# Performance work log

Hardware: AMD Instinct MI355X
Metric: run time of the kernel (lower is better)

The kernel has to match this reference:

```python
import jax, jax.numpy as jnp
import numpy as np

BITS = 4
NPACK = 32 // BITS            # 8 nibbles per int32
GROUPSIZE = 128
IN_F = 8192
OUT_F = 8192
BATCH = 64
NGROUPS = IN_F // GROUPSIZE   # 64
MASK = (1 << BITS) - 1        # 15


def setup_inputs() -> dict:
    key = jax.random.key(0)
    k1, k2, k3, k4, k5 = jax.random.split(key, 5)
    x = jax.random.normal(k1, (BATCH, IN_F), dtype=jnp.float32)
    qweight = jax.random.randint(k2, (IN_F // NPACK, OUT_F), 0, 2**31 - 1, dtype=jnp.int32)
    qzeros = jax.random.randint(k3, (NGROUPS, OUT_F // NPACK), 0, 2**31 - 1, dtype=jnp.int32)
    scales = jax.random.uniform(k4, (NGROUPS, OUT_F), dtype=jnp.float32, minval=1e-3, maxval=1e-2)
    bias = jax.random.normal(k5, (OUT_F,), dtype=jnp.float32)
    return {"x": x, "qweight": qweight, "qzeros": qzeros, "scales": scales, "bias": bias}


def _dequantize(qweight, qzeros, scales):
    shifts = (jnp.arange(NPACK, dtype=jnp.int32) * BITS)
    # unpack weight nibbles along in_features: [in/8, 8, out] -> [in, out]
    w = (qweight[:, None, :] >> shifts[None, :, None]) & MASK
    w = w.reshape(IN_F, OUT_F).astype(jnp.float32)
    # unpack zero points along out_features: [g, out/8, 8] -> [g, out]
    zp = (qzeros[:, :, None] >> shifts[None, None, :]) & MASK
    zp = zp.reshape(NGROUPS, OUT_F) + 1                       # optimum format stores zp-1
    zp = jnp.where(zp > MASK, 0, zp).astype(jnp.float32)      # wraparound per recover()
    g_idx = jnp.arange(IN_F) // GROUPSIZE                     # per-input-channel group id
    return (w - zp[g_idx]) * scales[g_idx]                    # [in, out] fp weight


def reference(x, qweight, qzeros, scales, bias):
    W = _dequantize(qweight, qzeros, scales)                  # [in, out]
    return x @ W + bias                                       # F.linear(x, W.T, bias)
```

## Files before the change

kernel.cpp:

```cpp
#include <hip/hip_runtime.h>
#include <hip/hip_bf16.h>

#define IN_F 8192
#define OUT_F 8192
#define BATCH 64
#define KSPLIT 16

typedef __attribute__((ext_vector_type(8))) _Float16 f16x8_t;
typedef __attribute__((ext_vector_type(2))) _Float16 f16x2_t;
typedef __attribute__((ext_vector_type(8))) ushort   u16x8_t;
typedef __attribute__((ext_vector_type(4))) float    f32x4_t;

__global__ void __launch_bounds__(512, 4)
wol_mfma(const float*  __restrict__ x,
         const int*    __restrict__ qw,
         const int*    __restrict__ qz,
         const float*  __restrict__ sc,
         ushort*       __restrict__ part) {
    const int nt   = blockIdx.x & 31;
    const int ks   = blockIdx.x >> 5;
    const int wid  = threadIdx.x >> 6;
    const int lane = threadIdx.x & 63;
    const int ln   = lane & 15;
    const int kb   = lane >> 4;
    const int colbase = nt * 256 + wid * 32;
    const int k0      = ks * 512;
    const int gbase   = k0 >> 7;
    const int qrowb   = k0 >> 3;

    unsigned qc[4][2]; float svc[2]; unsigned zwc[2];
#pragma unroll
    for (int kt = 0; kt < 4; ++kt)
#pragma unroll
        for (int nj = 0; nj < 2; ++nj)
            qc[kt][nj] = (unsigned)qw[(size_t)(qrowb + kt * 4 + kb) * OUT_F +
                                      colbase + nj * 16 + ln];
#pragma unroll
    for (int nj = 0; nj < 2; ++nj) {
        const int c = colbase + nj * 16 + ln;
        svc[nj] = sc[gbase * OUT_F + c];
        zwc[nj] = (unsigned)qz[gbase * (OUT_F / 8) + (c >> 3)];
    }
    __builtin_amdgcn_sched_barrier(0);

    __shared__ ushort lds_x[64 * 64 * 8];
    {
        const int perm[8] = {0, 4, 1, 5, 2, 6, 3, 7};
#pragma unroll
        for (int i = 0; i < 8; ++i) {
            const int idx = i * 512 + (int)threadIdx.x;
            const int row = idx >> 6;
            const int k8l = idx & 63;
            const float4* sp = (const float4*)&x[(size_t)row * IN_F + k0 + k8l * 8];
            const float4 a = sp[0], b = sp[1];
            const float f[8] = {a.x, a.y, a.z, a.w, b.x, b.y, b.z, b.w};
            union { ushort u[8]; u16x8_t v; } o;
#pragma unroll
            for (int j = 0; j < 8; ++j) {
                const _Float16 h = (_Float16)f[perm[j]];
                o.u[j] = *(const ushort*)&h;
            }
            unsigned byteoff = (unsigned)(row * 1024 + k8l * 16);
            byteoff ^= (unsigned)((row & 7) << 4);
            *(u16x8_t*)((char*)lds_x + byteoff) = o.v;
        }
    }
    __syncthreads();

    const unsigned xorv = (unsigned)((ln & 7) << 4);

    f32x4_t acc[4][2];
#pragma unroll
    for (int mi = 0; mi < 4; ++mi)
#pragma unroll
        for (int nj = 0; nj < 2; ++nj) acc[mi][nj] = (f32x4_t)0.0f;

#pragma unroll 1
    for (int g = 0; g < 4; ++g) {
        unsigned qn[4][2]; float svn[2]; unsigned zwn[2];
        if (g < 3) {
            const int qrow1 = qrowb + (g + 1) * 16;
#pragma unroll
            for (int kt = 0; kt < 4; ++kt)
#pragma unroll
                for (int nj = 0; nj < 2; ++nj)
                    qn[kt][nj] = (unsigned)qw[(size_t)(qrow1 + kt * 4 + kb) * OUT_F +
                                              colbase + nj * 16 + ln];
#pragma unroll
            for (int nj = 0; nj < 2; ++nj) {
                const int c = colbase + nj * 16 + ln;
                svn[nj] = sc[(gbase + g + 1) * OUT_F + c];
                zwn[nj] = (unsigned)qz[(gbase + g + 1) * (OUT_F / 8) + (c >> 3)];
            }
            __builtin_amdgcn_sched_barrier(0);
        }

        f16x2_t c2[2], s2[2];
#pragma unroll
        for (int nj = 0; nj < 2; ++nj) {
            const unsigned zp = ((zwc[nj] >> ((ln & 7) * 4)) + 1u) & 15u;
            const _Float16 hc = (_Float16)(-(float)(1024u + zp));
            const _Float16 hs = (_Float16)svc[nj];
            c2[nj][0] = hc; c2[nj][1] = hc;
            s2[nj][0] = hs; s2[nj][1] = hs;
        }

#pragma unroll
        for (int kt = 0; kt < 4; ++kt) {
            const unsigned kbyte = (unsigned)(g * 256 + kt * 64 + kb * 16) ^ xorv;
            f16x8_t af[4];
#pragma unroll
            for (int mi = 0; mi < 4; ++mi)
                af[mi] = *(const f16x8_t*)((const char*)lds_x +
                            (unsigned)((mi * 16 + ln) * 1024) + kbyte);
#pragma unroll
            for (int nj = 0; nj < 2; ++nj) {
                const unsigned qv = qc[kt][nj];
                const unsigned r0 = ( qv        & 0x000F000Fu) | 0x64006400u;
                const unsigned r1 = ((qv >> 4)  & 0x000F000Fu) | 0x64006400u;
                const unsigned r2 = ((qv >> 8)  & 0x000F000Fu) | 0x64006400u;
                const unsigned r3 = ((qv >> 12) & 0x000F000Fu) | 0x64006400u;
                union { unsigned u[4]; f16x8_t v; } bu;
                union { unsigned u; f16x2_t h; } t0, t1, t2, t3;
                t0.u = r0; t1.u = r1; t2.u = r2; t3.u = r3;
                f16x2_t w0 = (t0.h + c2[nj]) * s2[nj];
                f16x2_t w1 = (t1.h + c2[nj]) * s2[nj];
                f16x2_t w2 = (t2.h + c2[nj]) * s2[nj];
                f16x2_t w3 = (t3.h + c2[nj]) * s2[nj];
                bu.u[0] = *(const unsigned*)&w0;
                bu.u[1] = *(const unsigned*)&w1;
                bu.u[2] = *(const unsigned*)&w2;
                bu.u[3] = *(const unsigned*)&w3;
#pragma unroll
                for (int mi = 0; mi < 4; ++mi)
                    acc[mi][nj] = __builtin_amdgcn_mfma_f32_16x16x32_f16(
                        af[mi], bu.v, acc[mi][nj], 0, 0, 0);
            }
        }

        if (g < 3) {
#pragma unroll
            for (int kt = 0; kt < 4; ++kt)
#pragma unroll
                for (int nj = 0; nj < 2; ++nj) qc[kt][nj] = qn[kt][nj];
#pragma unroll
            for (int nj = 0; nj < 2; ++nj) { svc[nj] = svn[nj]; zwc[nj] = zwn[nj]; }
        }
    }

    union { ushort u[32]; u16x8_t v8[4]; } ob;
#pragma unroll
    for (int mi = 0; mi < 4; ++mi)
#pragma unroll
        for (int nj = 0; nj < 2; ++nj)
#pragma unroll
            for (int j = 0; j < 4; ++j) {
                __hip_bfloat16 h = __float2bfloat16(acc[mi][nj][j]);
                ob.u[(mi * 2 + nj) * 4 + j] = *reinterpret_cast<ushort*>(&h);
            }
    u16x8_t* pb = (u16x8_t*)part + ((size_t)(ks * 32 + nt) * 512 + threadIdx.x) * 4;
#pragma unroll
    for (int i = 0; i < 4; ++i) pb[i] = ob.v8[i];
}

__global__ void __launch_bounds__(256)
wol_reduce(const ushort* __restrict__ part,
           const float*  __restrict__ bias,
           float* __restrict__ out) {
    const int u   = blockIdx.x * 256 + threadIdx.x;
    const int v8  = u & 3;
    const int tid = (u >> 2) & 511;
    const int nt  = u >> 11;

    float s[8];
#pragma unroll
    for (int e = 0; e < 8; ++e) s[e] = 0.0f;
#pragma unroll
    for (int ks = 0; ks < KSPLIT; ++ks) {
        const u16x8_t p = *((const u16x8_t*)part +
                            (((size_t)(ks * 32 + nt) * 512 + tid) * 4 + v8));
#pragma unroll
        for (int e = 0; e < 8; ++e) {
            union { unsigned b; float f; } cv;
            cv.b = ((unsigned)(ushort)p[e]) << 16;
            s[e] += cv.f;
        }
    }

    const int wid = tid >> 6, lane = tid & 63;
    const int ln = lane & 15, kb = lane >> 4;
#pragma unroll
    for (int e = 0; e < 8; ++e) {
        const int idx = v8 * 8 + e;
        const int mi = idx >> 3, nj = (idx >> 2) & 1, j = idx & 3;
        const int row = mi * 16 + kb * 4 + j;
        const int col = nt * 256 + wid * 32 + nj * 16 + ln;
        out[(size_t)row * OUT_F + col] = s[e] + bias[col];
    }
}

extern "C" void kernel_launch(void* const* d_in, const int* in_sizes, int n_in,
                              void* d_out, int out_size, void* d_ws, size_t ws_size,
                              hipStream_t stream) {
    const float* x    = (const float*)d_in[0];
    const int*   qw   = (const int*)d_in[1];
    const int*   qz   = (const int*)d_in[2];
    const float* sc   = (const float*)d_in[3];
    const float* bias = (const float*)d_in[4];
    float* out = (float*)d_out;

    ushort* prt = (ushort*)d_ws;

    (void)in_sizes; (void)n_in; (void)ws_size; (void)out_size;

    wol_mfma<<<512, 512, 0, stream>>>(x, qw, qz, sc, prt);
    wol_reduce<<<256, 256, 0, stream>>>(prt, bias, out);
}
```

Measured before the change: 26.88 us.

## Stage packed weights into LDS via async global_load_lds instead of register prefetch

Packed int4 weights for the whole 512-row K slice are now loaded directly into a swizzled LDS buffer with global_load_lds, instead of being prefetched group by group into registers. All four groups' scales and zero words are loaded up front, and the group loop is fully unrolled. The aim is to issue every weight load at kernel start and overlap it with the x conversion, removing the per-group register double buffering. The cost is 64KB more LDS (128KB total), so launch bounds drop to 2 blocks per SM, which lowers occupancy and adds LDS read traffic for weights.

```diff
diff --git a/kernel.cpp b/kernel.cpp
--- a/kernel.cpp
+++ b/kernel.cpp
@@ -11,7 +11,10 @@
 typedef __attribute__((ext_vector_type(8))) ushort   u16x8_t;
 typedef __attribute__((ext_vector_type(4))) float    f32x4_t;
 
-__global__ void __launch_bounds__(512, 4)
+typedef const __attribute__((address_space(1))) unsigned gu32;
+typedef __attribute__((address_space(3))) unsigned       lu32;
+
+__global__ void __launch_bounds__(512, 2)
 wol_mfma(const float*  __restrict__ x,
          const int*    __restrict__ qw,
          const int*    __restrict__ qz,
@@ -28,22 +31,28 @@
     const int gbase   = k0 >> 7;
     const int qrowb   = k0 >> 3;
 
-    unsigned qc[4][2]; float svc[2]; unsigned zwc[2];
-#pragma unroll
-    for (int kt = 0; kt < 4; ++kt)
-#pragma unroll
-        for (int nj = 0; nj < 2; ++nj)
-            qc[kt][nj] = (unsigned)qw[(size_t)(qrowb + kt * 4 + kb) * OUT_F +
-                                      colbase + nj * 16 + ln];
-#pragma unroll
-    for (int nj = 0; nj < 2; ++nj) {
-        const int c = colbase + nj * 16 + ln;
-        svc[nj] = sc[gbase * OUT_F + c];
-        zwc[nj] = (unsigned)qz[gbase * (OUT_F / 8) + (c >> 3)];
-    }
-    __builtin_amdgcn_sched_barrier(0);
-
-    __shared__ ushort lds_x[64 * 64 * 8];
+    __shared__ ushort lds_x[64 * 512];
+    __shared__ int    lds_q[64 * 256];
+
+    float sv[4][2]; unsigned zw[4][2];
+#pragma unroll
+    for (int g = 0; g < 4; ++g)
+#pragma unroll
+        for (int nj = 0; nj < 2; ++nj) {
+            const int c = colbase + nj * 16 + ln;
+            sv[g][nj] = sc[(gbase + g) * OUT_F + c];
+            zw[g][nj] = (unsigned)qz[(gbase + g) * (OUT_F / 8) + (c >> 3)];
+        }
+
+#pragma unroll
+    for (int i = 0; i < 8; ++i) {
+        const int r   = wid * 8 + i;
+        const unsigned chunk = (unsigned)lane ^ (unsigned)((r & 3) << 1);
+        const int* gp = qw + (size_t)(qrowb + r) * OUT_F + nt * 256 + chunk * 4;
+        __builtin_amdgcn_global_load_lds((gu32*)gp, (lu32*)&lds_q[r * 256],
+                                         16, 0, 0);
+    }
+
     {
         const int perm[8] = {0, 4, 1, 5, 2, 6, 3, 7};
 #pragma unroll
@@ -68,6 +77,13 @@
     __syncthreads();
 
     const unsigned xorv = (unsigned)((ln & 7) << 4);
+    unsigned qb[2];
+#pragma unroll
+    for (int nj = 0; nj < 2; ++nj) {
+        const int col = wid * 32 + nj * 16 + ln;
+        qb[nj] = ((((unsigned)(col >> 2)) ^ (unsigned)(kb << 1)) << 4) +
+                 (unsigned)((ln & 3) * 4) + (unsigned)(kb * 1024);
+    }
 
     f32x4_t acc[4][2];
 #pragma unroll
@@ -75,32 +91,14 @@
 #pragma unroll
         for (int nj = 0; nj < 2; ++nj) acc[mi][nj] = (f32x4_t)0.0f;
 
-#pragma unroll 1
+#pragma unroll
     for (int g = 0; g < 4; ++g) {
-        unsigned qn[4][2]; float svn[2]; unsigned zwn[2];
-        if (g < 3) {
-            const int qrow1 = qrowb + (g + 1) * 16;
-#pragma unroll
-            for (int kt = 0; kt < 4; ++kt)
-#pragma unroll
-                for (int nj = 0; nj < 2; ++nj)
-                    qn[kt][nj] = (unsigned)qw[(size_t)(qrow1 + kt * 4 + kb) * OUT_F +
-                                              colbase + nj * 16 + ln];
-#pragma unroll
-            for (int nj = 0; nj < 2; ++nj) {
-                const int c = colbase + nj * 16 + ln;
-                svn[nj] = sc[(gbase + g + 1) * OUT_F + c];
-                zwn[nj] = (unsigned)qz[(gbase + g + 1) * (OUT_F / 8) + (c >> 3)];
-            }
-            __builtin_amdgcn_sched_barrier(0);
-        }
-
         f16x2_t c2[2], s2[2];
 #pragma unroll
         for (int nj = 0; nj < 2; ++nj) {
-            const unsigned zp = ((zwc[nj] >> ((ln & 7) * 4)) + 1u) & 15u;
+            const unsigned zp = ((zw[g][nj] >> ((ln & 7) * 4)) + 1u) & 15u;
             const _Float16 hc = (_Float16)(-(float)(1024u + zp));
-            const _Float16 hs = (_Float16)svc[nj];
+            const _Float16 hs = (_Float16)sv[g][nj];
             c2[nj][0] = hc; c2[nj][1] = hc;
             s2[nj][0] = hs; s2[nj][1] = hs;
         }
@@ -115,7 +113,8 @@
                             (unsigned)((mi * 16 + ln) * 1024) + kbyte);
 #pragma unroll
             for (int nj = 0; nj < 2; ++nj) {
-                const unsigned qv = qc[kt][nj];
+                const unsigned qv = *(const unsigned*)((const char*)lds_q +
+                                     qb[nj] + (unsigned)((g * 16 + kt * 4) * 1024));
                 const unsigned r0 = ( qv        & 0x000F000Fu) | 0x64006400u;
                 const unsigned r1 = ((qv >> 4)  & 0x000F000Fu) | 0x64006400u;
                 const unsigned r2 = ((qv >> 8)  & 0x000F000Fu) | 0x64006400u;
@@ -137,15 +136,6 @@
                         af[mi], bu.v, acc[mi][nj], 0, 0, 0);
             }
         }
-
-        if (g < 3) {
-#pragma unroll
-            for (int kt = 0; kt < 4; ++kt)
-#pragma unroll
-                for (int nj = 0; nj < 2; ++nj) qc[kt][nj] = qn[kt][nj];
-#pragma unroll
-            for (int nj = 0; nj < 2; ++nj) { svc[nj] = svn[nj]; zwc[nj] = zwn[nj]; }
-        }
     }
 
     union { ushort u[32]; u16x8_t v8[4]; } ob;
```

Measured after the change: 32.69 us. 1.22x slower.
